# Kernel optimization log

Hardware: AMD Instinct MI355X
Metric: run time of the kernel (lower is better)

## Reference

```python
import jax, jax.numpy as jnp
import numpy as np

N_NODES = 100000
N_EDGES = 640000
D_FEAT = 128
N_HIDDEN = 32


def setup_inputs() -> dict:
    key = jax.random.key(0)
    ks = jax.random.split(key, 8)
    x = jax.random.normal(ks[0], (N_NODES, D_FEAT), dtype=jnp.float32)
    edge_index = jax.random.randint(ks[1], (2, N_EDGES), 0, N_NODES, dtype=jnp.int64)
    # Glorot-ish scaled params
    W1_l = jax.random.normal(ks[2], (D_FEAT, N_HIDDEN), dtype=jnp.float32) / np.sqrt(D_FEAT)
    W1_r = jax.random.normal(ks[3], (D_FEAT, N_HIDDEN), dtype=jnp.float32) / np.sqrt(D_FEAT)
    b1 = jnp.zeros((N_HIDDEN,), dtype=jnp.float32)
    W2_l = jax.random.normal(ks[4], (N_HIDDEN, 1), dtype=jnp.float32) / np.sqrt(N_HIDDEN)
    W2_r = jax.random.normal(ks[5], (N_HIDDEN, 1), dtype=jnp.float32) / np.sqrt(N_HIDDEN)
    b2 = jnp.zeros((1,), dtype=jnp.float32)
    return {"x": x, "edge_index": edge_index, "W1_l": W1_l, "W1_r": W1_r,
            "b1": b1, "W2_l": W2_l, "W2_r": W2_r, "b2": b2}


def _sage_conv(h, src, dst, n_nodes, W_l, W_r, b):
    # mean aggregation of source features at destination nodes (PyG SAGEConv default)
    msg_sum = jax.ops.segment_sum(h[src], dst, num_segments=n_nodes)          # [N, d]
    deg = jax.ops.segment_sum(jnp.ones_like(src, dtype=h.dtype), dst,
                              num_segments=n_nodes)                           # [N]
    mean = msg_sum / jnp.maximum(deg, 1.0)[:, None]
    return mean @ W_l + h @ W_r + b


def reference(x, edge_index, W1_l, W1_r, b1, W2_l, W2_r, b2):
    src, dst = edge_index[0], edge_index[1]
    n = x.shape[0]
    h = jax.nn.relu(_sage_conv(x, src, dst, n, W1_l, W1_r, b1))
    # dropout p=0.1 is identity at inference (training=False)
    out = _sage_conv(h, src, dst, n, W2_l, W2_r, b2)
    return out  # [N, 1] node logits
```

## Files before the change

### kernel.cpp

```cpp
#include <hip/hip_runtime.h>

#define NN 100000
#define NE 640000
#define DF 128
#define NH 32
#define CAP 32
#define BINS 1563
#define HBLK 256
#define EPB 2500
#define QPB 625
#define NTILE 6250
#define GEMMB 391

typedef __attribute__((ext_vector_type(8))) short bf16x8;
typedef __attribute__((ext_vector_type(4))) float f32x4;

__device__ __forceinline__ unsigned short f2bf(float x) {
    union { float f; unsigned u; } c; c.f = x;
    unsigned r = c.u + 0x7fffu + ((c.u >> 16) & 1u);
    return (unsigned short)(r >> 16);
}
__device__ __forceinline__ float bf2f(unsigned short b) {
    union { unsigned u; float f; } c; c.u = ((unsigned)b) << 16;
    return c.f;
}

__global__ __launch_bounds__(256) void gemm_sort_kernel(
    const float* __restrict__ x, const float* __restrict__ W1_l,
    const float* __restrict__ W1_r, unsigned short* __restrict__ xl_bf,
    unsigned short* __restrict__ xr_bf, const int* __restrict__ src,
    const int* __restrict__ dst, int2* __restrict__ packmat,
    int* __restrict__ binned)
{
    __shared__ unsigned short wl[8192];
    __shared__ int lpart[256];

    if (blockIdx.x < HBLK) {
        int* lhist = (int*)wl;
        const int h = blockIdx.x;
        const int t = threadIdx.x;
        const int e0 = h * EPB;
        const int4* dq = (const int4*)(dst + e0);
        const int4* sq = (const int4*)(src + e0);
        for (int b = t; b < BINS; b += 256) lhist[b] = 0;
        __syncthreads();
        for (int q = t; q < QPB; q += 256) {
            int4 d4 = dq[q];
            atomicAdd(&lhist[d4.x >> 6], 1);
            atomicAdd(&lhist[d4.y >> 6], 1);
            atomicAdd(&lhist[d4.z >> 6], 1);
            atomicAdd(&lhist[d4.w >> 6], 1);
        }
        __syncthreads();
        const int k0 = t * 7, k1 = (k0 + 7 < BINS) ? k0 + 7 : BINS;
        int s = 0;
        for (int k = k0; k < k1; k++) s += lhist[k];
        lpart[t] = s;
        __syncthreads();
        for (int off = 1; off < 256; off <<= 1) {
            int v = (t >= off) ? lpart[t - off] : 0;
            __syncthreads();
            lpart[t] += v;
            __syncthreads();
        }
        int run = lpart[t] - s;
        for (int k = k0; k < k1; k++) {
            int c = lhist[k];
            packmat[(size_t)h * BINS + k] = make_int2(run, c);
            lhist[k] = run;
            run += c;
        }
        __syncthreads();
        for (int q = t; q < QPB; q += 256) {
            int4 d4 = dq[q];
            int4 s4 = sq[q];
#pragma unroll
            for (int i = 0; i < 4; i++) {
                int d = (&d4.x)[i], sv = (&s4.x)[i];
                int pos = atomicAdd(&lhist[d >> 6], 1);
                binned[e0 + pos] = (sv << 6) | (d & 63);
            }
        }
        return;
    }

    for (int s = threadIdx.x; s < 1024; s += 256) {
        int lane = s & 63;
        int nt = (s >> 6) & 3;
        int ks = s >> 8;
        int n = nt * 16 + (lane & 15);
        const float* Wc = (n < 32) ? (W1_l + n) : (W1_r + (n - 32));
        unsigned short v[8];
#pragma unroll
        for (int i = 0; i < 8; i++) {
            int k = ks * 32 + ((i >> 2) << 4) + ((lane >> 4) << 2) + (i & 3);
            v[i] = f2bf(Wc[(size_t)k * 32]);
        }
        unsigned u0 = (unsigned)v[0] | ((unsigned)v[1] << 16);
        unsigned u1 = (unsigned)v[2] | ((unsigned)v[3] << 16);
        unsigned u2 = (unsigned)v[4] | ((unsigned)v[5] << 16);
        unsigned u3 = (unsigned)v[6] | ((unsigned)v[7] << 16);
        *(uint4*)&wl[s * 8] = make_uint4(u0, u1, u2, u3);
    }
    __syncthreads();

    const int lane = threadIdx.x & 63;
    const int wslot = ((blockIdx.x - HBLK) << 2) + (threadIdx.x >> 6);
    const int m = lane & 15, g = lane >> 4;

#define BLOAD(ks, nt) const bf16x8 b##ks##nt = *(const bf16x8*)&wl[(((ks)*4 + (nt)) * 64 + lane) * 8];
    BLOAD(0,0) BLOAD(0,1) BLOAD(0,2) BLOAD(0,3)
    BLOAD(1,0) BLOAD(1,1) BLOAD(1,2) BLOAD(1,3)
    BLOAD(2,0) BLOAD(2,1) BLOAD(2,2) BLOAD(2,3)
    BLOAD(3,0) BLOAD(3,1) BLOAD(3,2) BLOAD(3,3)
#undef BLOAD

#pragma unroll
    for (int tt = 0; tt < 4; tt++) {
        const int tile = wslot * 4 + tt;
        if (tile >= NTILE) break;
        const int row0 = tile << 4;
        const float* xp = x + (size_t)(row0 + m) * DF + g * 4;

        f32x4 acc0 = {0.f,0.f,0.f,0.f}, acc1 = {0.f,0.f,0.f,0.f};
        f32x4 acc2 = {0.f,0.f,0.f,0.f}, acc3 = {0.f,0.f,0.f,0.f};

#define KSTEP(ks) { \
        float4 fa = *(const float4*)(xp + (ks) * 32); \
        float4 fb = *(const float4*)(xp + (ks) * 32 + 16); \
        bf16x8 af; \
        af[0] = (short)f2bf(fa.x); af[1] = (short)f2bf(fa.y); \
        af[2] = (short)f2bf(fa.z); af[3] = (short)f2bf(fa.w); \
        af[4] = (short)f2bf(fb.x); af[5] = (short)f2bf(fb.y); \
        af[6] = (short)f2bf(fb.z); af[7] = (short)f2bf(fb.w); \
        acc0 = __builtin_amdgcn_mfma_f32_16x16x32_bf16(af, b##ks##0, acc0, 0, 0, 0); \
        acc1 = __builtin_amdgcn_mfma_f32_16x16x32_bf16(af, b##ks##1, acc1, 0, 0, 0); \
        acc2 = __builtin_amdgcn_mfma_f32_16x16x32_bf16(af, b##ks##2, acc2, 0, 0, 0); \
        acc3 = __builtin_amdgcn_mfma_f32_16x16x32_bf16(af, b##ks##3, acc3, 0, 0, 0); }
        KSTEP(0) KSTEP(1) KSTEP(2) KSTEP(3)
#undef KSTEP

#define CSTORE(nt) { \
        int n = (nt) * 16 + m; \
_Pragma("unroll") \
        for (int r = 0; r < 4; r++) { \
            int rr = row0 + g * 4 + r; \
            unsigned short v = f2bf(acc##nt[r]); \
            if (n < 32) xl_bf[(size_t)rr * 32 + n] = v; \
            else        xr_bf[(size_t)rr * 32 + (n - 32)] = v; \
        } }
        CSTORE(0) CSTORE(1) CSTORE(2) CSTORE(3)
#undef CSTORE
    }
}

__global__ __launch_bounds__(256) void agg1_bin_kernel(
    const int* __restrict__ binned, const int2* __restrict__ packmat,
    const unsigned short* __restrict__ xl_bf, const unsigned short* __restrict__ xr_bf,
    const float* __restrict__ b1, const float* __restrict__ W2_l,
    const float* __restrict__ W2_r, float* __restrict__ h2l, float* __restrict__ hrp)
{
    __shared__ int lcnt[64];
    __shared__ int lesrc[64 * CAP];
    const int j = blockIdx.x, t = threadIdx.x;
    int2 sc = packmat[(size_t)t * BINS + j];
    if (t < 64) lcnt[t] = 0;
    __syncthreads();

    {
        const int base = t * EPB + sc.x;
        for (int k = 0; k < sc.y; k++) {
            int pk = binned[base + k];
            int dl = pk & 63, s = pk >> 6;
            int p = atomicAdd(&lcnt[dl], 1);
            if (p < CAP) lesrc[(dl << 5) + p] = s;
        }
    }
    __syncthreads();

    const int l = t & 31, grp = t >> 5;
    const int j8 = l >> 2, c = l & 3;
    const float4* b14 = (const float4*)&b1[c * 8];
    float4 bb0 = b14[0], bb1 = b14[1];
    const float4* wl4 = (const float4*)&W2_l[c * 8];
    float4 wl0 = wl4[0], wl1 = wl4[1];
    const float4* wr4 = (const float4*)&W2_r[c * 8];
    float4 wr0 = wr4[0], wr1 = wr4[1];
    const float bs[8]  = {bb0.x, bb0.y, bb0.z, bb0.w, bb1.x, bb1.y, bb1.z, bb1.w};
    const float wls[8] = {wl0.x, wl0.y, wl0.z, wl0.w, wl1.x, wl1.y, wl1.z, wl1.w};
    const float wrs[8] = {wr0.x, wr0.y, wr0.z, wr0.w, wr1.x, wr1.y, wr1.z, wr1.w};

    for (int dl = grp; dl < 64; dl += 8) {
        const int node = j * 64 + dl;
        if (node >= NN) break;
        const int dg = lcnt[dl];
        const int lim = (dg < CAP) ? dg : CAP;

        float acc[8];
#pragma unroll
        for (int i = 0; i < 8; i++) acc[i] = 0.f;

        for (int jb = 0; jb < lim; jb += 8) {
            int jj = jb + j8;
            if (jj < lim) {
                int s = lesrc[(dl << 5) + jj];
                uint4 v = *(const uint4*)&xl_bf[(size_t)s * NH + c * 8];
#pragma unroll
                for (int i = 0; i < 4; i++) {
                    unsigned u = (&v.x)[i];
                    acc[2 * i]     += bf2f((unsigned short)(u & 0xffffu));
                    acc[2 * i + 1] += bf2f((unsigned short)(u >> 16));
                }
            }
        }
#pragma unroll
        for (int mm = 4; mm <= 16; mm <<= 1)
#pragma unroll
            for (int i = 0; i < 8; i++) acc[i] += __shfl_xor(acc[i], mm);

        const float inv = 1.0f / fmaxf((float)dg, 1.0f);
        uint4 xv = *(const uint4*)&xr_bf[(size_t)node * NH + c * 8];
        float sl = 0.f, sr = 0.f;
#pragma unroll
        for (int i = 0; i < 4; i++) {
            unsigned u = (&xv.x)[i];
            float xlo = bf2f((unsigned short)(u & 0xffffu));
            float xhi = bf2f((unsigned short)(u >> 16));
            float h0 = fmaxf(fmaf(acc[2 * i],     inv, xlo + bs[2 * i]),     0.f);
            float h1 = fmaxf(fmaf(acc[2 * i + 1], inv, xhi + bs[2 * i + 1]), 0.f);
            sl = fmaf(h0, wls[2 * i], sl); sl = fmaf(h1, wls[2 * i + 1], sl);
            sr = fmaf(h0, wrs[2 * i], sr); sr = fmaf(h1, wrs[2 * i + 1], sr);
        }
        sl += __shfl_xor(sl, 1); sl += __shfl_xor(sl, 2);
        sr += __shfl_xor(sr, 1); sr += __shfl_xor(sr, 2);
        if (l == 0) {
            h2l[node] = sl;
            hrp[node] = sr;
        }
    }
}

__global__ __launch_bounds__(256) void agg2_bin_kernel(
    const int* __restrict__ binned, const int2* __restrict__ packmat,
    const float* __restrict__ h2l, const float* __restrict__ hrp,
    const float* __restrict__ b2, float* __restrict__ out)
{
    __shared__ float lsum[64];
    __shared__ int lcc[64];
    const int j = blockIdx.x, t = threadIdx.x;
    int2 sc = packmat[(size_t)t * BINS + j];
    if (t < 64) { lsum[t] = 0.f; lcc[t] = 0; }
    __syncthreads();
    {
        const int base = t * EPB + sc.x;
        for (int k = 0; k < sc.y; k++) {
            int pk = binned[base + k];
            int dl = pk & 63, s = pk >> 6;
            atomicAdd(&lsum[dl], h2l[s]);
            atomicAdd(&lcc[dl], 1);
        }
    }
    __syncthreads();
    if (t < 64) {
        int node = j * 64 + t;
        if (node < NN)
            out[node] = lsum[t] / fmaxf((float)lcc[t], 1.0f) + hrp[node] + b2[0];
    }
}

extern "C" void kernel_launch(void* const* d_in, const int* in_sizes, int n_in,
                              void* d_out, int out_size, void* d_ws, size_t ws_size,
                              hipStream_t stream)
{
    const float* x    = (const float*)d_in[0];
    const int*   ei   = (const int*)d_in[1];
    const float* W1_l = (const float*)d_in[2];
    const float* W1_r = (const float*)d_in[3];
    const float* b1   = (const float*)d_in[4];
    const float* W2_l = (const float*)d_in[5];
    const float* W2_r = (const float*)d_in[6];
    const float* b2   = (const float*)d_in[7];
    float* out = (float*)d_out;

    const int* src = ei;
    const int* dst = ei + NE;

    unsigned short* xl_bf = (unsigned short*)d_ws;
    unsigned short* xr_bf = xl_bf + (size_t)NN * NH;
    float* h2l      = (float*)(xr_bf + (size_t)NN * NH);
    float* hrp      = h2l + NN;
    int2*  packmat  = (int2*)(hrp + NN);
    int*   binned   = (int*)(packmat + (size_t)HBLK * BINS);

    gemm_sort_kernel<<<HBLK + GEMMB, 256, 0, stream>>>(x, W1_l, W1_r, xl_bf, xr_bf,
                                                       src, dst, packmat, binned);
    agg1_bin_kernel<<<BINS, 256, 0, stream>>>(binned, packmat, xl_bf, xr_bf,
                                              b1, W2_l, W2_r, h2l, hrp);
    agg2_bin_kernel<<<BINS, 256, 0, stream>>>(binned, packmat, h2l, hrp, b2, out);
}
```

Before: 67.37 us.

## Fuse layer-2 aggregation into agg1 via source-binned global atomic scatter

The sort phase now builds a second edge binning keyed by source node, alongside the destination binning, and zeroes a global accumulator. After agg1 computes each node's layer-2 left projection in shared memory, it scatters that value with global float atomics to the destination nodes of its outgoing edges. A tiny final kernel then divides by the saved in-degree and adds the right-hand term and bias. This drops the separate agg2 pass, which gathered random h2l values. In exchange it adds a second sort pass and 640k random global atomics. GEMM blocks are also doubled, with each wave handling two tiles instead of four.

```diff
diff --git a/kernel.cpp b/kernel.cpp
--- a/kernel.cpp
+++ b/kernel.cpp
@@ -10,7 +10,7 @@
 #define EPB 2500
 #define QPB 625
 #define NTILE 6250
-#define GEMMB 391
+#define GEMMB 782
 
 typedef __attribute__((ext_vector_type(8))) short bf16x8;
 typedef __attribute__((ext_vector_type(4))) float f32x4;
@@ -29,27 +29,40 @@
     const float* __restrict__ x, const float* __restrict__ W1_l,
     const float* __restrict__ W1_r, unsigned short* __restrict__ xl_bf,
     unsigned short* __restrict__ xr_bf, const int* __restrict__ src,
-    const int* __restrict__ dst, int2* __restrict__ packmat,
-    int* __restrict__ binned)
+    const int* __restrict__ dst,
+    int2* __restrict__ packmat,  int* __restrict__ binned,
+    int2* __restrict__ packmat2, int* __restrict__ binned2,
+    float4* __restrict__ acc4)
 {
     __shared__ unsigned short wl[8192];
     __shared__ int lpart[256];
 
-    if (blockIdx.x < HBLK) {
+    if (blockIdx.x < 2 * HBLK) {
+        const int role = (blockIdx.x >= HBLK);
+        const int h = blockIdx.x - (role ? HBLK : 0);
+        const int t = threadIdx.x;
+        const int* keys = role ? src : dst;
+        const int* vals = role ? dst : src;
+        int2* pm = role ? packmat2 : packmat;
+        int*  bn = role ? binned2  : binned;
+
+        if (!role) {
+            int gi = h * 256 + t;
+            if (gi < NN / 4) acc4[gi] = make_float4(0.f, 0.f, 0.f, 0.f);
+        }
+
         int* lhist = (int*)wl;
-        const int h = blockIdx.x;
-        const int t = threadIdx.x;
         const int e0 = h * EPB;
-        const int4* dq = (const int4*)(dst + e0);
-        const int4* sq = (const int4*)(src + e0);
+        const int4* kq = (const int4*)(keys + e0);
+        const int4* vq = (const int4*)(vals + e0);
         for (int b = t; b < BINS; b += 256) lhist[b] = 0;
         __syncthreads();
         for (int q = t; q < QPB; q += 256) {
-            int4 d4 = dq[q];
-            atomicAdd(&lhist[d4.x >> 6], 1);
-            atomicAdd(&lhist[d4.y >> 6], 1);
-            atomicAdd(&lhist[d4.z >> 6], 1);
-            atomicAdd(&lhist[d4.w >> 6], 1);
+            int4 k4 = kq[q];
+            atomicAdd(&lhist[k4.x >> 6], 1);
+            atomicAdd(&lhist[k4.y >> 6], 1);
+            atomicAdd(&lhist[k4.z >> 6], 1);
+            atomicAdd(&lhist[k4.w >> 6], 1);
         }
         __syncthreads();
         const int k0 = t * 7, k1 = (k0 + 7 < BINS) ? k0 + 7 : BINS;
@@ -66,19 +79,19 @@
         int run = lpart[t] - s;
         for (int k = k0; k < k1; k++) {
             int c = lhist[k];
-            packmat[(size_t)h * BINS + k] = make_int2(run, c);
+            pm[(size_t)h * BINS + k] = make_int2(run, c);
             lhist[k] = run;
             run += c;
         }
         __syncthreads();
         for (int q = t; q < QPB; q += 256) {
-            int4 d4 = dq[q];
-            int4 s4 = sq[q];
+            int4 k4 = kq[q];
+            int4 v4 = vq[q];
 #pragma unroll
             for (int i = 0; i < 4; i++) {
-                int d = (&d4.x)[i], sv = (&s4.x)[i];
-                int pos = atomicAdd(&lhist[d >> 6], 1);
-                binned[e0 + pos] = (sv << 6) | (d & 63);
+                int kk = (&k4.x)[i], vv = (&v4.x)[i];
+                int pos = atomicAdd(&lhist[kk >> 6], 1);
+                bn[e0 + pos] = (vv << 6) | (kk & 63);
             }
         }
         return;
@@ -105,7 +118,7 @@
     __syncthreads();
 
     const int lane = threadIdx.x & 63;
-    const int wslot = ((blockIdx.x - HBLK) << 2) + (threadIdx.x >> 6);
+    const int wslot = ((blockIdx.x - 2 * HBLK) << 2) + (threadIdx.x >> 6);
     const int m = lane & 15, g = lane >> 4;
 
 #define BLOAD(ks, nt) const bf16x8 b##ks##nt = *(const bf16x8*)&wl[(((ks)*4 + (nt)) * 64 + lane) * 8];
@@ -116,8 +129,8 @@
 #undef BLOAD
 
 #pragma unroll
-    for (int tt = 0; tt < 4; tt++) {
-        const int tile = wslot * 4 + tt;
+    for (int tt = 0; tt < 2; tt++) {
+        const int tile = wslot * 2 + tt;
         if (tile >= NTILE) break;
         const int row0 = tile << 4;
         const float* xp = x + (size_t)(row0 + m) * DF + g * 4;
@@ -154,16 +167,20 @@
     }
 }
 
-__global__ __launch_bounds__(256) void agg1_bin_kernel(
+__global__ __launch_bounds__(256) void agg1_kernel(
     const int* __restrict__ binned, const int2* __restrict__ packmat,
+    const int* __restrict__ binned2, const int2* __restrict__ packmat2,
     const unsigned short* __restrict__ xl_bf, const unsigned short* __restrict__ xr_bf,
     const float* __restrict__ b1, const float* __restrict__ W2_l,
-    const float* __restrict__ W2_r, float* __restrict__ h2l, float* __restrict__ hrp)
+    const float* __restrict__ W2_r, float* __restrict__ hrp,
+    int* __restrict__ deg, float* __restrict__ acc_out)
 {
     __shared__ int lcnt[64];
     __shared__ int lesrc[64 * CAP];
+    __shared__ float lsl[64];
     const int j = blockIdx.x, t = threadIdx.x;
-    int2 sc = packmat[(size_t)t * BINS + j];
+    int2 sc  = packmat [(size_t)t * BINS + j];
+    int2 sc2 = packmat2[(size_t)t * BINS + j];
     if (t < 64) lcnt[t] = 0;
     __syncthreads();
 
@@ -177,6 +194,10 @@
         }
     }
     __syncthreads();
+    if (t < 64) {
+        int node = j * 64 + t;
+        if (node < NN) deg[node] = lcnt[t];
+    }
 
     const int l = t & 31, grp = t >> 5;
     const int j8 = l >> 2, c = l & 3;
@@ -234,38 +255,29 @@
         sl += __shfl_xor(sl, 1); sl += __shfl_xor(sl, 2);
         sr += __shfl_xor(sr, 1); sr += __shfl_xor(sr, 2);
         if (l == 0) {
-            h2l[node] = sl;
+            lsl[dl] = sl;
             hrp[node] = sr;
         }
     }
-}
-
-__global__ __launch_bounds__(256) void agg2_bin_kernel(
-    const int* __restrict__ binned, const int2* __restrict__ packmat,
-    const float* __restrict__ h2l, const float* __restrict__ hrp,
-    const float* __restrict__ b2, float* __restrict__ out)
+    __syncthreads();
+
+    {
+        const int base2 = t * EPB + sc2.x;
+        for (int k = 0; k < sc2.y; k++) {
+            int pk = binned2[base2 + k];
+            atomicAdd(&acc_out[pk >> 6], lsl[pk & 63]);
+        }
+    }
+}
+
+__global__ __launch_bounds__(256) void final_kernel(
+    const float* __restrict__ acc, const int* __restrict__ deg,
+    const float* __restrict__ hrp, const float* __restrict__ b2,
+    float* __restrict__ out)
 {
-    __shared__ float lsum[64];
-    __shared__ int lcc[64];
-    const int j = blockIdx.x, t = threadIdx.x;
-    int2 sc = packmat[(size_t)t * BINS + j];
-    if (t < 64) { lsum[t] = 0.f; lcc[t] = 0; }
-    __syncthreads();
-    {
-        const int base = t * EPB + sc.x;
-        for (int k = 0; k < sc.y; k++) {
-            int pk = binned[base + k];
-            int dl = pk & 63, s = pk >> 6;
-            atomicAdd(&lsum[dl], h2l[s]);
-            atomicAdd(&lcc[dl], 1);
-        }
-    }
-    __syncthreads();
-    if (t < 64) {
-        int node = j * 64 + t;
-        if (node < NN)
-            out[node] = lsum[t] / fmaxf((float)lcc[t], 1.0f) + hrp[node] + b2[0];
-    }
+    int i = blockIdx.x * 256 + threadIdx.x;
+    if (i < NN)
+        out[i] = acc[i] / fmaxf((float)deg[i], 1.0f) + hrp[i] + b2[0];
 }
 
 extern "C" void kernel_launch(void* const* d_in, const int* in_sizes, int n_in,
@@ -287,14 +299,19 @@
 
     unsigned short* xl_bf = (unsigned short*)d_ws;
     unsigned short* xr_bf = xl_bf + (size_t)NN * NH;
-    float* h2l      = (float*)(xr_bf + (size_t)NN * NH);
-    float* hrp      = h2l + NN;
-    int2*  packmat  = (int2*)(hrp + NN);
-    int*   binned   = (int*)(packmat + (size_t)HBLK * BINS);
-
-    gemm_sort_kernel<<<HBLK + GEMMB, 256, 0, stream>>>(x, W1_l, W1_r, xl_bf, xr_bf,
-                                                       src, dst, packmat, binned);
-    agg1_bin_kernel<<<BINS, 256, 0, stream>>>(binned, packmat, xl_bf, xr_bf,
-                                              b1, W2_l, W2_r, h2l, hrp);
-    agg2_bin_kernel<<<BINS, 256, 0, stream>>>(binned, packmat, h2l, hrp, b2, out);
-}
+    float* hrp      = (float*)(xr_bf + (size_t)NN * NH);
+    float* acc      = hrp + NN;
+    int*   deg      = (int*)(acc + NN);
+    int2*  packmat  = (int2*)(deg + NN);
+    int2*  packmat2 = packmat + (size_t)HBLK * BINS;
+    int*   binned   = (int*)(packmat2 + (size_t)HBLK * BINS);
+    int*   binned2  = binned + NE;
+
+    gemm_sort_kernel<<<2 * HBLK + GEMMB, 256, 0, stream>>>(
+        x, W1_l, W1_r, xl_bf, xr_bf, src, dst,
+        packmat, binned, packmat2, binned2, (float4*)acc);
+    agg1_kernel<<<BINS, 256, 0, stream>>>(binned, packmat, binned2, packmat2,
+                                          xl_bf, xr_bf, b1, W2_l, W2_r,
+                                          hrp, deg, acc);
+    final_kernel<<<(NN + 255) / 256, 256, 0, stream>>>(acc, deg, hrp, b2, out);
+}
```

Result: slower. 88.65 us (+31.6%).
